# Kernel tuning notes

Hardware: AMD Instinct MI355X
Metric: run time of the kernel (lower is better)

## Reference

```python
import math
import jax, jax.numpy as jnp
import numpy as np

NUM_HEADS = 16
WINDOW = 64  # neighbor_size
NEG_INF = -1e30


def setup_inputs() -> dict:
    key = jax.random.key(0)
    ks = jax.random.split(key, 5)
    B, L, D = 2, 2048, 1024
    x = jax.random.normal(ks[0], (B, L, D), dtype=jnp.float32)
    s = 0.02
    Wq = jax.random.normal(ks[1], (D, D), dtype=jnp.float32) * s
    Wk = jax.random.normal(ks[2], (D, D), dtype=jnp.float32) * s
    Wv = jax.random.normal(ks[3], (D, D), dtype=jnp.float32) * s
    Wo = jax.random.normal(ks[4], (D, D), dtype=jnp.float32) * s
    return {
        "x": x, "Wq": Wq, "Wk": Wk, "Wv": Wv, "Wo": Wo,
        "sep_gate": jnp.float32(0.1),
        "align_gate": jnp.float32(0.1),
        "coh_gate": jnp.float32(0.1),
    }


def reference(x, Wq, Wk, Wv, Wo, sep_gate, align_gate, coh_gate):
    B, L, D = x.shape
    H = NUM_HEADS
    hd = D // H
    scale = math.sqrt(hd)

    # projections (torch Linear: y = x @ W.T), split heads -> (B, H, L, hd)
    def proj(W):
        return (x @ W.T).reshape(B, L, H, hd).transpose(0, 2, 1, 3)

    q, k, v = proj(Wq), proj(Wk), proj(Wv)

    # raw scores (B, H, L, L)
    scores = jnp.einsum("bhqd,bhkd->bhqk", q, k) / scale

    # Reynolds rules (applied BEFORE masking, mean over full kv dim, as in source)
    similarity = jax.nn.sigmoid(scores)
    separation = -sep_gate * similarity ** 2
    alignment = align_gate * scores
    score_mean = jnp.mean(scores, axis=-1, keepdims=True)
    cohesion = -coh_gate * jnp.abs(scores - score_mean)
    scores = scores + separation + alignment + cohesion

    # causal sliding-window mask: attend iff 0 <= i - j < WINDOW
    i = jnp.arange(L)[:, None]
    j = jnp.arange(L)[None, :]
    dist = i - j
    masked = (dist < 0) | (dist >= WINDOW)  # (L, L) True = blocked
    scores = jnp.where(masked[None, None, :, :], NEG_INF, scores)

    attn = jax.nn.softmax(scores, axis=-1)  # dropout p=0.0 -> identity
    out = jnp.einsum("bhqk,bhkd->bhqd", attn, v)
    out = out.transpose(0, 2, 1, 3).reshape(B, L, D)
    return out @ Wo.T
```

## Files before the change

kernel.cpp:

```cpp
#include <hip/hip_runtime.h>
#include <math.h>

#define L_SEQ 2048
#define DMODEL 1024
#define HEADS 16
#define HD 64
#define BATCH 2
#define MROWS (BATCH*L_SEQ)
#define KDIM 1024
#define VSTRIDE 2136

typedef short bfrag8 __attribute__((ext_vector_type(8)));
typedef float f32x4f __attribute__((ext_vector_type(4)));

__device__ __forceinline__ unsigned short f2bf(float f) {
    unsigned u = __float_as_uint(f);
    unsigned r = u + 0x7FFFu + ((u >> 16) & 1u);
    return (unsigned short)(r >> 16);
}
__device__ __forceinline__ float bf2f(unsigned short h) {
    return __uint_as_float(((unsigned)h) << 16);
}

__global__ __launch_bounds__(256) void convert_bf16(
    const float* __restrict__ x, const float* __restrict__ wq,
    const float* __restrict__ wk, const float* __restrict__ wv,
    const float* __restrict__ wo,
    unsigned short* __restrict__ xb, unsigned short* __restrict__ qwb,
    unsigned short* __restrict__ kwb, unsigned short* __restrict__ vwb,
    unsigned short* __restrict__ owb, float* __restrict__ kmean_acc)
{
    const int bid = blockIdx.x;
    if (bid == 8192) {
        float4 z = make_float4(0.f, 0.f, 0.f, 0.f);
        *(float4*)&kmean_acc[threadIdx.x * 8]     = z;
        *(float4*)&kmean_acc[threadIdx.x * 8 + 4] = z;
        return;
    }
    const float* src; unsigned short* dst; size_t base;
    if (bid < 4096) { src = x; dst = xb; base = (size_t)bid * 1024; }
    else {
        const int r = bid - 4096; const int w = r >> 10; const int off = r & 1023;
        src = (w==0) ? wq : (w==1) ? wk : (w==2) ? wv : wo;
        dst = (w==0) ? qwb : (w==1) ? kwb : (w==2) ? vwb : owb;
        base = (size_t)off * 1024;
    }
    const size_t idx = base + (size_t)threadIdx.x * 4;
    float4 v = *(const float4*)&src[idx];
    ushort4 o;
    o.x = f2bf(v.x); o.y = f2bf(v.y); o.z = f2bf(v.z); o.w = f2bf(v.w);
    *(ushort4*)&dst[idx] = o;
}

#define GBK 64

template<int MODE>
__global__ void mfma_gemm(
    const unsigned short* __restrict__ A,
    const unsigned short* __restrict__ W0, const unsigned short* __restrict__ W1,
    const unsigned short* __restrict__ W2,
    void* __restrict__ C0v, void* __restrict__ C1v, void* __restrict__ C2v,
    float* __restrict__ kmean_acc)
{
    __shared__ short As[128*GBK];
    __shared__ short Bs[128*GBK];

    const int tid  = threadIdx.x;
    const int wave = tid >> 6, lane = tid & 63;
    const int m0   = blockIdx.x * 128;
    const int n0g  = blockIdx.y * 128;

    const unsigned short* Wp; int n0; int which = 0;
    if (MODE == 1) {
        which = n0g >> 10;
        n0 = n0g & 1023;
        Wp = (which==0) ? W0 : (which==1) ? W1 : W2;
    } else { n0 = n0g; Wp = W0; }

    const int quad = lane >> 4, lm = lane & 15;
    const int wm = wave >> 1, wn = wave & 1;

    f32x4f acc[4][4] = {};

    const int se   = wave * 2048 + lane * 8;
    const int srow = se >> 6;
    const int scg  = (se & 63) >> 3;
    const int sgcol = ((scg ^ (srow & 7)) << 3);

    for (int k0 = 0; k0 < KDIM; k0 += GBK) {
        __syncthreads();
        #pragma unroll
        for (int i = 0; i < 4; ++i) {
            const int ebase = wave * 2048 + i * 512;
            const int row = srow + i * 8;
            __builtin_amdgcn_global_load_lds(
                (const __attribute__((address_space(1))) void*)(A + (size_t)(m0 + row) * KDIM + k0 + sgcol),
                (__attribute__((address_space(3))) void*)(&As[ebase]), 16, 0, 0);
            __builtin_amdgcn_global_load_lds(
                (const __attribute__((address_space(1))) void*)(Wp + (size_t)(n0 + row) * KDIM + k0 + sgcol),
                (__attribute__((address_space(3))) void*)(&Bs[ebase]), 16, 0, 0);
        }
        __syncthreads();

        #pragma unroll
        for (int kk = 0; kk < 2; ++kk) {
            bfrag8 af[4], bf[4];
            #pragma unroll
            for (int t = 0; t < 4; ++t) {
                const int ar = wm*64 + t*16 + lm;
                af[t] = *(const bfrag8*)&As[ar*GBK + (((kk*4 + quad) ^ (ar & 7)) << 3)];
                const int br = wn*64 + t*16 + lm;
                bf[t] = *(const bfrag8*)&Bs[br*GBK + (((kk*4 + quad) ^ (br & 7)) << 3)];
            }
            #pragma unroll
            for (int mt = 0; mt < 4; ++mt)
                #pragma unroll
                for (int nt = 0; nt < 4; ++nt)
                    acc[mt][nt] = __builtin_amdgcn_mfma_f32_16x16x32_bf16(
                        af[mt], bf[nt], acc[mt][nt], 0, 0, 0);
        }
    }

    if (MODE == 1) {
        if (which == 2) {
            unsigned short* Vp = (unsigned short*)C2v;
            #pragma unroll
            for (int mt = 0; mt < 4; ++mt)
                #pragma unroll
                for (int nt = 0; nt < 4; ++nt) {
                    const int gn = n0 + wn*64 + nt*16 + lm;
                    const int h = gn >> 6, d = gn & 63;
                    const int gm0 = m0 + wm*64 + mt*16 + quad*4;
                    const int b = gm0 >> 11, l0 = gm0 & (L_SEQ-1);
                    ushort4 o;
                    o.x = f2bf(acc[mt][nt][0]); o.y = f2bf(acc[mt][nt][1]);
                    o.z = f2bf(acc[mt][nt][2]); o.w = f2bf(acc[mt][nt][3]);
                    *(ushort4*)&Vp[((size_t)((b*HEADS + h)*HD + d))*VSTRIDE + 64 + l0] = o;
                }
        } else {
            unsigned short* Cp = (unsigned short*)((which==0) ? C0v : C1v);
            #pragma unroll
            for (int mt = 0; mt < 4; ++mt)
                #pragma unroll
                for (int nt = 0; nt < 4; ++nt) {
                    const int gn = n0 + wn*64 + nt*16 + lm;
                    const int h = gn >> 6, d = gn & 63;
                    #pragma unroll
                    for (int r = 0; r < 4; ++r) {
                        const int gm = m0 + wm*64 + mt*16 + quad*4 + r;
                        const int b = gm >> 11, l = gm & (L_SEQ-1);
                        Cp[(((size_t)(b*HEADS + h) * L_SEQ) + l) * HD + d] = f2bf(acc[mt][nt][r]);
                    }
                }
            if (which == 1) {
                const int b = m0 >> 11;
                #pragma unroll
                for (int nt = 0; nt < 4; ++nt) {
                    const int gn = n0 + wn*64 + nt*16 + lm;
                    const int h = gn >> 6, d = gn & 63;
                    float s = 0.f;
                    #pragma unroll
                    for (int mt = 0; mt < 4; ++mt)
                        #pragma unroll
                        for (int r = 0; r < 4; ++r) s += acc[mt][nt][r];
                    atomicAdd(&kmean_acc[(size_t)(b*HEADS + h)*HD + d], s);
                }
            }
        }
    } else {
        float* Cp = (float*)C0v;
        #pragma unroll
        for (int mt = 0; mt < 4; ++mt)
            #pragma unroll
            for (int nt = 0; nt < 4; ++nt) {
                const int gn = n0 + wn*64 + nt*16 + lm;
                #pragma unroll
                for (int r = 0; r < 4; ++r) {
                    const int gm = m0 + wm*64 + mt*16 + quad*4 + r;
                    Cp[(size_t)gm * DMODEL + gn] = acc[mt][nt][r];
                }
            }
    }
}

#define P_STRIDE 104

__global__ __launch_bounds__(256) void attn_kernel(
    const unsigned short* __restrict__ qb, const unsigned short* __restrict__ kb,
    const unsigned short* __restrict__ vt, const float* __restrict__ kmean_acc,
    const float* __restrict__ g_sep, const float* __restrict__ g_align,
    const float* __restrict__ g_coh, unsigned short* __restrict__ out)
{
    __shared__ unsigned short pl[64 * P_STRIDE];

    const int tid = threadIdx.x;
    const int bh = blockIdx.x >> 5;
    const int qt = blockIdx.x & 31;
    const int q0 = qt * 64;
    const int j0 = q0 - 64;

    const int w = tid >> 6, lane = tid & 63;
    const int quad = lane >> 4, lm = lane & 15;
    const float sep = g_sep[0], align = g_align[0], coh = g_coh[0];

    const unsigned short* kbh = kb + (size_t)bh * L_SEQ * HD;
    const unsigned short* vbh = vt + (size_t)bh * HD * VSTRIDE;

    const unsigned short* qrow =
        qb + ((size_t)bh * L_SEQ + q0 + w*16 + lm) * HD + quad * 8;
    bfrag8 qa0 = *(const bfrag8*)qrow;
    bfrag8 qa1 = *(const bfrag8*)(qrow + 32);

    const float* kmp = kmean_acc + bh * HD + quad * 8;
    float4 km0 = *(const float4*)(kmp);
    float4 km1 = *(const float4*)(kmp + 4);
    float4 km2 = *(const float4*)(kmp + 32);
    float4 km3 = *(const float4*)(kmp + 36);
    float part =
        bf2f((unsigned short)qa0[0])*km0.x + bf2f((unsigned short)qa0[1])*km0.y +
        bf2f((unsigned short)qa0[2])*km0.z + bf2f((unsigned short)qa0[3])*km0.w +
        bf2f((unsigned short)qa0[4])*km1.x + bf2f((unsigned short)qa0[5])*km1.y +
        bf2f((unsigned short)qa0[6])*km1.z + bf2f((unsigned short)qa0[7])*km1.w +
        bf2f((unsigned short)qa1[0])*km2.x + bf2f((unsigned short)qa1[1])*km2.y +
        bf2f((unsigned short)qa1[2])*km2.z + bf2f((unsigned short)qa1[3])*km2.w +
        bf2f((unsigned short)qa1[4])*km3.x + bf2f((unsigned short)qa1[5])*km3.y +
        bf2f((unsigned short)qa1[6])*km3.z + bf2f((unsigned short)qa1[7])*km3.w;
    part *= (1.f / (float)L_SEQ);
    part += __shfl_xor(part, 16, 64);
    part += __shfl_xor(part, 32, 64);

    f32x4f sacc[6];
    #pragma unroll
    for (int t = 0; t < 6; ++t) {
        int kr = j0 + w*16 + t*16 + lm;
        kr = kr < 0 ? 0 : (kr >= L_SEQ ? L_SEQ - 1 : kr);
        const unsigned short* kp = kbh + (size_t)kr * HD + quad * 8;
        bfrag8 b0 = *(const bfrag8*)kp;
        bfrag8 b1 = *(const bfrag8*)(kp + 32);
        f32x4f z = {0.f, 0.f, 0.f, 0.f};
        z = __builtin_amdgcn_mfma_f32_16x16x32_bf16(qa0, b0, z, 0, 0, 0);
        sacc[t] = __builtin_amdgcn_mfma_f32_16x16x32_bf16(qa1, b1, z, 0, 0, 0);
    }

    float rinv[4];
    #pragma unroll
    for (int r = 0; r < 4; ++r) {
        const int row = quad*4 + r;
        const int i   = q0 + w*16 + row;
        const float mean_i = __shfl(part, row, 64) * 0.125f;
        float sc[6]; float mx = -3.0e38f;
        #pragma unroll
        for (int t = 0; t < 6; ++t) {
            const int jabs = j0 + w*16 + t*16 + lm;
            const int dist = i - jabs;
            float s = sacc[t][r] * 0.125f;
            const float sig = 1.f / (1.f + __expf(-s));
            float adj = s * (1.f + align) - sep * sig * sig - coh * fabsf(s - mean_i);
            const bool ok = (dist >= 0) && (dist < 64) && (jabs >= 0);
            sc[t] = ok ? adj : -3.0e38f;
            mx = fmaxf(mx, sc[t]);
        }
        mx = fmaxf(mx, __shfl_xor(mx, 1, 64));
        mx = fmaxf(mx, __shfl_xor(mx, 2, 64));
        mx = fmaxf(mx, __shfl_xor(mx, 4, 64));
        mx = fmaxf(mx, __shfl_xor(mx, 8, 64));
        float ls = 0.f;
        #pragma unroll
        for (int t = 0; t < 6; ++t) {
            const float p = __expf(sc[t] - mx);
            ls += p;
            pl[(w*16 + row) * P_STRIDE + t*16 + lm] = f2bf(p);
        }
        ls += __shfl_xor(ls, 1, 64);
        ls += __shfl_xor(ls, 2, 64);
        ls += __shfl_xor(ls, 4, 64);
        ls += __shfl_xor(ls, 8, 64);
        rinv[r] = 1.f / ls;
    }

    f32x4f oacc[4] = {};
    #pragma unroll
    for (int kk = 0; kk < 3; ++kk) {
        bfrag8 pa = *(const bfrag8*)&pl[(w*16 + lm) * P_STRIDE + kk*32 + quad*8];
        const int loff = 64 + j0 + w*16 + kk*32 + quad*8;
        #pragma unroll
        for (int nt = 0; nt < 4; ++nt) {
            bfrag8 bv = *(const bfrag8*)&vbh[(size_t)(nt*16 + lm) * VSTRIDE + loff];
            oacc[nt] = __builtin_amdgcn_mfma_f32_16x16x32_bf16(pa, bv, oacc[nt], 0, 0, 0);
        }
    }

    const int b = bh >> 4, h = bh & (HEADS - 1);
    #pragma unroll
    for (int nt = 0; nt < 4; ++nt)
        #pragma unroll
        for (int r = 0; r < 4; ++r) {
            const int i = q0 + w*16 + quad*4 + r;
            const int d = nt*16 + lm;
            out[((size_t)(b * L_SEQ + i)) * DMODEL + h * HD + d] =
                f2bf(oacc[nt][r] * rinv[r]);
        }
}

extern "C" void kernel_launch(void* const* d_in, const int* in_sizes, int n_in,
                              void* d_out, int out_size, void* d_ws, size_t ws_size,
                              hipStream_t stream)
{
    (void)in_sizes; (void)n_in; (void)out_size; (void)ws_size;
    const float* x     = (const float*)d_in[0];
    const float* Wq    = (const float*)d_in[1];
    const float* Wk    = (const float*)d_in[2];
    const float* Wv    = (const float*)d_in[3];
    const float* Wo    = (const float*)d_in[4];
    const float* g_sep   = (const float*)d_in[5];
    const float* g_align = (const float*)d_in[6];
    const float* g_coh   = (const float*)d_in[7];
    float* out = (float*)d_out;

    float* kmean_ws = (float*)d_ws;
    unsigned short* xb  = (unsigned short*)(kmean_ws + 2048);
    const size_t per = (size_t)MROWS * DMODEL;
    unsigned short* wqb = xb  + per;
    unsigned short* wkb = wqb + (size_t)DMODEL*KDIM;
    unsigned short* wvb = wkb + (size_t)DMODEL*KDIM;
    unsigned short* wob = wvb + (size_t)DMODEL*KDIM;
    unsigned short* qb  = wob + (size_t)DMODEL*KDIM;
    unsigned short* kb  = qb  + per;
    unsigned short* vtb = kb  + per;
    unsigned short* attb = vtb + (size_t)BATCH*HEADS*HD*VSTRIDE;

    convert_bf16<<<dim3(8193), dim3(256), 0, stream>>>(
        x, Wq, Wk, Wv, Wo, xb, wqb, wkb, wvb, wob, kmean_ws);
    mfma_gemm<1><<<dim3(MROWS/128, 3*DMODEL/128), dim3(256), 0, stream>>>(
        xb, wqb, wkb, wvb, qb, kb, vtb, kmean_ws);
    attn_kernel<<<dim3(BATCH*HEADS*(L_SEQ/64)), dim3(256), 0, stream>>>(
        qb, kb, vtb, kmean_ws, g_sep, g_align, g_coh, attb);
    mfma_gemm<0><<<dim3(MROWS/128, DMODEL/128), dim3(256), 0, stream>>>(
        attb, wob, nullptr, nullptr, out, nullptr, nullptr, nullptr);
}
```

Before: 163.7 us.

## Prefetch next GEMM K-tile into registers instead of direct global-to-LDS loads

Result: slower. 276.9 us (+69.2%).

```diff
diff --git a/kernel.cpp b/kernel.cpp
--- a/kernel.cpp
+++ b/kernel.cpp
@@ -55,7 +55,7 @@
 #define GBK 64
 
 template<int MODE>
-__global__ void mfma_gemm(
+__global__ __launch_bounds__(256, 1) void mfma_gemm(
     const unsigned short* __restrict__ A,
     const unsigned short* __restrict__ W0, const unsigned short* __restrict__ W1,
     const unsigned short* __restrict__ W2,
@@ -82,23 +82,35 @@
 
     f32x4f acc[4][4] = {};
 
-    const int se   = wave * 2048 + lane * 8;
-    const int srow = se >> 6;
-    const int scg  = (se & 63) >> 3;
-    const int sgcol = ((scg ^ (srow & 7)) << 3);
+    const int e0    = wave * 2048 + lane * 8;
+    const int srow0 = e0 >> 6;
+    const int scol  = e0 & 63;
+    const int swz   = ((scol >> 3) ^ (srow0 & 7)) << 3;
+
+    const unsigned short* Aptr = A  + (size_t)(m0 + srow0) * KDIM + scol;
+    const unsigned short* Wptr = Wp + (size_t)(n0 + srow0) * KDIM + scol;
+
+    uint4 pa[4], pb[4];
+    #pragma unroll
+    for (int i = 0; i < 4; ++i) {
+        pa[i] = *(const uint4*)(Aptr + (size_t)(8*i) * KDIM);
+        pb[i] = *(const uint4*)(Wptr + (size_t)(8*i) * KDIM);
+    }
 
     for (int k0 = 0; k0 < KDIM; k0 += GBK) {
         __syncthreads();
         #pragma unroll
         for (int i = 0; i < 4; ++i) {
-            const int ebase = wave * 2048 + i * 512;
-            const int row = srow + i * 8;
-            __builtin_amdgcn_global_load_lds(
-                (const __attribute__((address_space(1))) void*)(A + (size_t)(m0 + row) * KDIM + k0 + sgcol),
-                (__attribute__((address_space(3))) void*)(&As[ebase]), 16, 0, 0);
-            __builtin_amdgcn_global_load_lds(
-                (const __attribute__((address_space(1))) void*)(Wp + (size_t)(n0 + row) * KDIM + k0 + sgcol),
-                (__attribute__((address_space(3))) void*)(&Bs[ebase]), 16, 0, 0);
+            const int off = (srow0 + 8*i) * GBK + swz;
+            *(uint4*)&As[off] = pa[i];
+            *(uint4*)&Bs[off] = pb[i];
+        }
+        if (k0 + GBK < KDIM) {
+            #pragma unroll
+            for (int i = 0; i < 4; ++i) {
+                pa[i] = *(const uint4*)(Aptr + (size_t)(8*i) * KDIM + k0 + GBK);
+                pb[i] = *(const uint4*)(Wptr + (size_t)(8*i) * KDIM + k0 + GBK);
+            }
         }
         __syncthreads();
 
```
